# Performance work log

Hardware: AMD Instinct MI355X
Metric: run time of the kernel (lower is better)

Reference implementation:

```python
import jax, jax.numpy as jnp
import numpy as np

WS = (7, 7)   # window size
SS = (3, 3)   # shift size
NH = 8        # num heads
DIM = 256
B_, H_, W_ = 16, 112, 112


def _rel_index(wh, ww):
    ch, cw = np.meshgrid(np.arange(wh), np.arange(ww), indexing='ij')
    cf = np.stack([ch, cw]).reshape(2, -1)
    rc = (cf[:, :, None] - cf[:, None, :]).transpose(1, 2, 0)
    rc[:, :, 0] += wh - 1
    rc[:, :, 1] += ww - 1
    rc[:, :, 0] *= 2 * ww - 1
    return rc.sum(-1).reshape(-1)


def _shift_mask(pH, pW, wh, ww, sh, sw):
    m = np.zeros((pH, pW))
    cnt = 0
    for h0, h1 in ((0, pH - wh), (pH - wh, pH - sh), (pH - sh, pH)):
        for w0, w1 in ((0, pW - ww), (pW - ww, pW - sw), (pW - sw, pW)):
            m[h0:h1, w0:w1] = cnt
            cnt += 1
    m = m.reshape(pH // wh, wh, pW // ww, ww).transpose(0, 2, 1, 3).reshape(-1, wh * ww)
    d = m[:, None, :] - m[:, :, None]  # (nW, N, N), [w,i,j] = m[w,j]-m[w,i]
    return np.where(d != 0, -100.0, 0.0).astype(np.float32)


def _partition(x, wh, ww):
    B, H, W, C = x.shape
    x = x.reshape(B, H // wh, wh, W // ww, ww, C).transpose(0, 1, 3, 2, 4, 5)
    return x.reshape(B * (H // wh) * (W // ww), wh * ww, C)


def _unpartition(x, B, H, W, wh, ww):
    C = x.shape[-1]
    x = x.reshape(B, H // wh, W // ww, wh, ww, C).transpose(0, 1, 3, 2, 4, 5)
    return x.reshape(B, H, W, C)


def setup_inputs() -> dict:
    key = jax.random.key(0)
    ks = jax.random.split(key, 12)
    D = DIM
    inp = {
        'Q': jax.random.normal(ks[0], (B_, H_, W_, D), jnp.float32),
        'K': jax.random.normal(ks[1], (B_, H_, W_, D), jnp.float32),
        'V': jax.random.normal(ks[2], (B_, H_, W_, D), jnp.float32),
        'Qw': jax.random.normal(ks[3], (D, D), jnp.float32) * 0.02,
        'Qb': jax.random.normal(ks[4], (D,), jnp.float32) * 0.02,
        'Kw': jax.random.normal(ks[5], (D, D), jnp.float32) * 0.02,
        'Kb': jax.random.normal(ks[6], (D,), jnp.float32) * 0.02,
        'Vw': jax.random.normal(ks[7], (D, D), jnp.float32) * 0.02,
        'Vb': jax.random.normal(ks[8], (D,), jnp.float32) * 0.02,
        'Pw': jax.random.normal(ks[9], (D, D), jnp.float32) * 0.02,
        'Pb': jax.random.normal(ks[10], (D,), jnp.float32) * 0.02,
        'rpb_table': jax.random.normal(ks[11], ((2 * WS[0] - 1) * (2 * WS[1] - 1), NH), jnp.float32) * 0.02,
        'rp_index': jnp.asarray(_rel_index(WS[0], WS[1]), jnp.int32),
    }
    return inp


def reference(Q, K, V, Qw, Qb, Kw, Kb, Vw, Vb, Pw, Pb, rpb_table, rp_index):
    wh, ww = WS
    nh = NH
    B, H, W, C = Q.shape
    N = wh * ww
    hd = C // nh
    pad_b = (wh - H % wh) % wh
    pad_r = (ww - W % ww) % ww
    if pad_b or pad_r:
        pad = ((0, 0), (0, pad_b), (0, pad_r), (0, 0))
        Q, K, V = jnp.pad(Q, pad), jnp.pad(K, pad), jnp.pad(V, pad)
    pH, pW = H + pad_b, W + pad_r
    sh = 0 if wh >= pH else SS[0]
    sw = 0 if ww >= pW else SS[1]
    shifted = (sh + sw) > 0
    if shifted:
        Q = jnp.roll(Q, (-sh, -sw), (1, 2))
        K = jnp.roll(K, (-sh, -sw), (1, 2))
        V = jnp.roll(V, (-sh, -sw), (1, 2))
    xq = _partition(Q, wh, ww)  # (B*nW, N, C)
    xk = _partition(K, wh, ww)
    xv = _partition(V, wh, ww)
    q = (xq @ Qw.T + Qb).reshape(-1, N, nh, hd).transpose(0, 2, 1, 3) * (hd ** -0.5)
    k = (xk @ Kw.T + Kb).reshape(-1, N, nh, hd).transpose(0, 2, 1, 3)
    v = (xv @ Vw.T + Vb).reshape(-1, N, nh, hd).transpose(0, 2, 1, 3)
    bias = rpb_table[rp_index].reshape(N, N, nh).transpose(2, 0, 1)  # (nh, N, N)
    attn = jnp.einsum('bhnd,bhmd->bhnm', q, k) + bias[None]
    if shifted:
        mask = jnp.asarray(_shift_mask(pH, pW, wh, ww, sh, sw))  # (nW, N, N)
        nW = (pH // wh) * (pW // ww)
        attn = attn.reshape(B, nW, nh, N, N) + mask[None, :, None]
        attn = attn.reshape(-1, nh, N, N)
    attn = jax.nn.softmax(attn, axis=-1)
    x = jnp.einsum('bhnm,bhmd->bhnd', attn, v).transpose(0, 2, 1, 3).reshape(-1, N, C)
    x = x @ Pw.T + Pb
    x = _unpartition(x, B, pH, pW, wh, ww)
    if shifted:
        x = jnp.roll(x, (sh, sw), (1, 2))
    return x[:, :H, :W, :]
```

## Files before the change

### kernel.cpp

```cpp
#include <hip/hip_runtime.h>


typedef short  bf16x4_t __attribute__((ext_vector_type(4)));
typedef short  bf16x8_t __attribute__((ext_vector_type(8)));
typedef float  f32x4_t  __attribute__((ext_vector_type(4)));
typedef int    i32x4_t  __attribute__((ext_vector_type(4)));

#define HH    112
#define WWDIM 112
#define NTOK  49
#define NWIN  4096
#define SHIFT 3
#define LOG2E 1.4426950408889634f
#define MASKS (-144.26950408889634f)

__device__ __forceinline__ unsigned short f2bf(float f) {
  unsigned u = __builtin_bit_cast(unsigned, f);
  u += 0x7FFFu + ((u >> 16) & 1u);
  return (unsigned short)(u >> 16);
}

__device__ __forceinline__ unsigned cvtpk(float a, float b) {
  unsigned r;
  asm("v_cvt_pk_bf16_f32 %0, %1, %2" : "=v"(r) : "v"(a), "v"(b));
  return r;
}

__device__ __forceinline__ float exp2fast(float x) {
  float r;
  asm("v_exp_f32 %0, %1" : "=v"(r) : "v"(x));
  return r;
}

__device__ __forceinline__ bf16x8_t ld8(const unsigned short* p) {
  return __builtin_bit_cast(bf16x8_t, *reinterpret_cast<const i32x4_t*>(p));
}

__device__ __forceinline__ bf16x4_t pack4(float a, float b, float c, float d) {
  union { unsigned u[2]; bf16x4_t v; } t;
  t.u[0] = cvtpk(a, b); t.u[1] = cvtpk(c, d);
  return t.v;
}

__device__ __forceinline__ int swzi(int row, int col, int rowElems) {
  int by = col << 1;
  int sb = (((by >> 4) ^ (row & 7)) << 4) | (by & 15);
  return row * rowElems + (sb >> 1);
}

__global__ void prep_kernel(const float* __restrict__ Qw, const float* __restrict__ Kw,
                            const float* __restrict__ Vw, const float* __restrict__ Pw,
                            const float* __restrict__ rpb, const int* __restrict__ rpi,
                            unsigned short* __restrict__ wbf, float* __restrict__ biasP) {
  int idx = blockIdx.x * 256 + threadIdx.x;
  if (idx < 4 * 65536) {
    int which = idx >> 16, e = idx & 65535;
    const float* s = (which == 0) ? Qw : (which == 1) ? Kw : (which == 2) ? Vw : Pw;
    wbf[idx] = f2bf(s[e]);
  }
  if (idx < 8 * 49 * 64) {
    int h = idx / 3136, r = idx - h * 3136;
    int i = r >> 6, j = r & 63;
    biasP[idx] = (i < NTOK && j < NTOK) ? rpb[rpi[i * NTOK + j] * 8 + h] * LOG2E : 0.f;
  }
}

#define GLOAD(SRC)                                                            \
  do {                                                                        \
    _Pragma("unroll") for (int it = 0; it < 8; ++it) {                        \
      g[it] = ((wid + (it << 3)) < NTOK)                                      \
                  ? *reinterpret_cast<const float4*>((SRC) + goff[it])        \
                  : make_float4(0.f, 0.f, 0.f, 0.f);                          \
    }                                                                         \
  } while (0)

#define XWRITE(B)                                                             \
  do {                                                                        \
    _Pragma("unroll") for (int it = 0; it < 8; ++it) {                        \
      unsigned v0 = cvtpk(g[it].x, g[it].y);                                  \
      unsigned v1 = cvtpk(g[it].z, g[it].w);                                  \
      *reinterpret_cast<uint2*>(                                              \
          &Xs[B][swzi(wid + (it << 3), lane << 2, 256)]) = make_uint2(v0, v1);\
    }                                                                         \
  } while (0)

#define WHOIST(PH)                                                            \
  do {                                                                        \
    const unsigned short* W_ = wbf + ((PH) << 16);                            \
    _Pragma("unroll") for (int ks = 0; ks < 8; ++ks)                          \
        _Pragma("unroll") for (int t = 0; t < 2; ++t)                         \
            bw[ks][t] =                                                       \
        ld8(&W_[(((wid << 5) + (t << 4) + lo) << 8) + (ks << 5) + kof]);      \
  } while (0)

__global__ __launch_bounds__(512, 2) void fused_kernel(
    const float* __restrict__ Qin, const float* __restrict__ Kin, const float* __restrict__ Vin,
    const float* __restrict__ Qbv, const float* __restrict__ Kbv, const float* __restrict__ Vbv,
    const float* __restrict__ Pbv,
    const unsigned short* __restrict__ wbf, const float* __restrict__ biasP,
    float* __restrict__ out) {
  __shared__ unsigned short Xs[2][64 * 256];

  const int blk = blockIdx.x, tid = threadIdx.x;
  const int lane = tid & 63, wid = tid >> 6;
  const int b = blk >> 8, wi = (blk >> 4) & 15, wj = blk & 15;
  const int lo = lane & 15, hi = lane >> 4;
  const int g4 = hi << 2, kof = hi << 3;

  unsigned goff[8];
#pragma unroll
  for (int it = 0; it < 8; ++it) {
    int row = wid + (it << 3);
    unsigned off = 0;
    if (row < NTOK) {
      int i = row / 7, j = row - i * 7;
      int h_ = wi * 7 + i + SHIFT; if (h_ >= HH) h_ -= HH;
      int w_ = wj * 7 + j + SHIFT; if (w_ >= WWDIM) w_ -= WWDIM;
      off = ((unsigned)((b * HH + h_) * WWDIM + w_) << 8) + (lane << 2);
    }
    goff[it] = off;
  }

  float4 g[8];
  bf16x8_t bw[8][2];
  bf16x4_t qf[2][4], kf[2][4], vf[4][2];

  GLOAD(Qin);
  XWRITE(0);
  WHOIST(0);
  __syncthreads();

#pragma unroll
  for (int ph = 0; ph < 2; ++ph) {
    GLOAD(ph == 0 ? Kin : Vin);
    const unsigned short* Xb = Xs[ph];
    f32x4_t acc[2][4];
#pragma unroll
    for (int a = 0; a < 2; ++a)
#pragma unroll
      for (int c = 0; c < 4; ++c) acc[a][c] = (f32x4_t){0.f, 0.f, 0.f, 0.f};
#pragma unroll
    for (int ks = 0; ks < 8; ++ks) {
      const int kk = (ks << 5) + kof;
      bf16x8_t xb[4];
#pragma unroll
      for (int nj = 0; nj < 4; ++nj) xb[nj] = ld8(&Xb[swzi((nj << 4) + lo, kk, 256)]);
#pragma unroll
      for (int mi = 0; mi < 2; ++mi)
#pragma unroll
        for (int nj = 0; nj < 4; ++nj)
          acc[mi][nj] = __builtin_amdgcn_mfma_f32_16x16x32_bf16(bw[ks][mi], xb[nj], acc[mi][nj], 0, 0, 0);
    }
    const float* bias = (ph == 0) ? Qbv : Kbv;
    const float scale = (ph == 0) ? 0.17677669529663687f * LOG2E : 1.0f;
    bf16x4_t (*dst)[4] = (ph == 0) ? qf : kf;
#pragma unroll
    for (int mi = 0; mi < 2; ++mi) {
      const float4 bb = *reinterpret_cast<const float4*>(bias + (wid << 5) + (mi << 4) + g4);
#pragma unroll
      for (int nj = 0; nj < 4; ++nj)
        dst[mi][nj] = pack4((acc[mi][nj][0] + bb.x) * scale, (acc[mi][nj][1] + bb.y) * scale,
                            (acc[mi][nj][2] + bb.z) * scale, (acc[mi][nj][3] + bb.w) * scale);
    }
    XWRITE(ph ^ 1);
    WHOIST(ph + 1);
    __syncthreads();
  }

  {
    const unsigned short* Xb = Xs[0];
    f32x4_t acc[4][2];
#pragma unroll
    for (int a = 0; a < 4; ++a)
#pragma unroll
      for (int c = 0; c < 2; ++c) acc[a][c] = (f32x4_t){0.f, 0.f, 0.f, 0.f};
#pragma unroll
    for (int ks = 0; ks < 8; ++ks) {
      const int kk = (ks << 5) + kof;
      bf16x8_t xa[4];
#pragma unroll
      for (int mi = 0; mi < 4; ++mi) xa[mi] = ld8(&Xb[swzi((mi << 4) + lo, kk, 256)]);
#pragma unroll
      for (int mi = 0; mi < 4; ++mi)
#pragma unroll
        for (int t = 0; t < 2; ++t)
          acc[mi][t] = __builtin_amdgcn_mfma_f32_16x16x32_bf16(xa[mi], bw[ks][t], acc[mi][t], 0, 0, 0);
    }
    float bbv[2];
#pragma unroll
    for (int t = 0; t < 2; ++t) bbv[t] = Vbv[(wid << 5) + (t << 4) + lo];
#pragma unroll
    for (int mi = 0; mi < 4; ++mi)
#pragma unroll
      for (int t = 0; t < 2; ++t)
        vf[mi][t] = pack4(acc[mi][t][0] + bbv[t], acc[mi][t][1] + bbv[t],
                          acc[mi][t][2] + bbv[t], acc[mi][t][3] + bbv[t]);
  }
  WHOIST(3);

  const bool wi15 = (wi == 15), wj15 = (wj == 15);
  unsigned kbi = 0, kbj = 0, kval = 0;
#pragma unroll
  for (int njk = 0; njk < 4; ++njk)
#pragma unroll
    for (int rg = 0; rg < 4; ++rg) {
      int kt = (njk << 4) + g4 + rg;
      if (kt < NTOK) {
        int ti = kt / 7, tj = kt - (kt / 7) * 7;
        unsigned bit = 1u << (njk * 4 + rg);
        kval |= bit;
        if (ti >= 4) kbi |= bit;
        if (tj >= 4) kbj |= bit;
      }
    }

  bf16x4_t pf[4][4];
#pragma unroll
  for (int njq = 0; njq < 4; ++njq) {
    const int qt = (njq << 4) + lo;
    const bool qv = qt < NTOK;
    const int sqt = qv ? qt : 0;
    const float* bq = biasP + wid * 3136 + (sqt << 6);
    f32x4_t bfr[4];
#pragma unroll
    for (int njk = 0; njk < 4; ++njk)
      bfr[njk] = *reinterpret_cast<const f32x4_t*>(bq + (njk << 4) + g4);

    f32x4_t stc[4];
    __builtin_amdgcn_s_setprio(1);
#pragma unroll
    for (int njk = 0; njk < 4; ++njk) {
      stc[njk] = __builtin_amdgcn_mfma_f32_16x16x16bf16_1k(
          kf[0][njk], qf[0][njq], (f32x4_t){0.f, 0.f, 0.f, 0.f}, 0, 0, 0);
      stc[njk] = __builtin_amdgcn_mfma_f32_16x16x16bf16_1k(
          kf[1][njk], qf[1][njq], stc[njk], 0, 0, 0);
    }
    __builtin_amdgcn_s_setprio(0);

    const int qti = sqt / 7, qtj = sqt - (sqt / 7) * 7;
    const bool qbi = qti >= 4, qbj = qtj >= 4;
    float vals[4][4];
    float m = -3e38f;
#pragma unroll
    for (int njk = 0; njk < 4; ++njk)
#pragma unroll
      for (int rg = 0; rg < 4; ++rg) {
        const int bit = njk * 4 + rg;
        const bool valid = qv && ((kval >> bit) & 1u);
        float v = stc[njk][rg] + bfr[njk][rg];
        if (wi15 && (qbi != (bool)((kbi >> bit) & 1u))) v += MASKS;
        if (wj15 && (qbj != (bool)((kbj >> bit) & 1u))) v += MASKS;
        v = valid ? v : -1e30f;
        vals[njk][rg] = v;
        m = fmaxf(m, v);
      }
    m = fmaxf(m, __shfl_xor(m, 16));
    m = fmaxf(m, __shfl_xor(m, 32));
    float sum = 0.f;
#pragma unroll
    for (int njk = 0; njk < 4; ++njk)
#pragma unroll
      for (int rg = 0; rg < 4; ++rg) {
        const float e = exp2fast(vals[njk][rg] - m);
        vals[njk][rg] = e;
        sum += e;
      }
    sum += __shfl_xor(sum, 16);
    sum += __shfl_xor(sum, 32);
    const float inv = __builtin_amdgcn_rcpf(sum);
#pragma unroll
    for (int njk = 0; njk < 4; ++njk)
      pf[njk][njq] = pack4(vals[njk][0] * inv, vals[njk][1] * inv,
                           vals[njk][2] * inv, vals[njk][3] * inv);
  }

  f32x4_t o[2][4];
#pragma unroll
  for (int a = 0; a < 2; ++a)
#pragma unroll
    for (int c = 0; c < 4; ++c) o[a][c] = (f32x4_t){0.f, 0.f, 0.f, 0.f};
  __builtin_amdgcn_s_setprio(1);
#pragma unroll
  for (int mi = 0; mi < 4; ++mi)
#pragma unroll
    for (int t = 0; t < 2; ++t)
#pragma unroll
      for (int njq = 0; njq < 4; ++njq)
        o[t][njq] = __builtin_amdgcn_mfma_f32_16x16x16bf16_1k(vf[mi][t], pf[mi][njq], o[t][njq], 0, 0, 0);
  __builtin_amdgcn_s_setprio(0);

#pragma unroll
  for (int t = 0; t < 2; ++t)
#pragma unroll
    for (int njq = 0; njq < 4; ++njq) {
      const int qt = (njq << 4) + lo;
      const int ch0 = (wid << 5) + (t << 4) + g4;
      *reinterpret_cast<uint2*>(&Xs[1][swzi(qt, ch0, 256)]) =
          make_uint2(cvtpk(o[t][njq][0], o[t][njq][1]), cvtpk(o[t][njq][2], o[t][njq][3]));
    }
  __syncthreads();

  {
    const unsigned short* Xb = Xs[1];
    f32x4_t y[2][4];
#pragma unroll
    for (int a = 0; a < 2; ++a)
#pragma unroll
      for (int c = 0; c < 4; ++c) y[a][c] = (f32x4_t){0.f, 0.f, 0.f, 0.f};
#pragma unroll
    for (int ks = 0; ks < 8; ++ks) {
      const int kk = (ks << 5) + kof;
      bf16x8_t xb[4];
#pragma unroll
      for (int nj = 0; nj < 4; ++nj) xb[nj] = ld8(&Xb[swzi((nj << 4) + lo, kk, 256)]);
#pragma unroll
      for (int mi = 0; mi < 2; ++mi)
#pragma unroll
        for (int nj = 0; nj < 4; ++nj)
          y[mi][nj] = __builtin_amdgcn_mfma_f32_16x16x32_bf16(bw[ks][mi], xb[nj], y[mi][nj], 0, 0, 0);
    }
    float4 pb[2];
#pragma unroll
    for (int mi = 0; mi < 2; ++mi)
      pb[mi] = *reinterpret_cast<const float4*>(Pbv + (wid << 5) + (mi << 4) + g4);
#pragma unroll
    for (int nj = 0; nj < 4; ++nj) {
      const int tok = (nj << 4) + lo;
      if (tok < NTOK) {
        const int i = tok / 7, j = tok - (tok / 7) * 7;
        int h_ = wi * 7 + i + SHIFT; if (h_ >= HH) h_ -= HH;
        int w_ = wj * 7 + j + SHIFT; if (w_ >= WWDIM) w_ -= WWDIM;
        float* ob = out + ((size_t)((b * HH + h_) * WWDIM + w_) << 8);
#pragma unroll
        for (int mi = 0; mi < 2; ++mi) {
          const int ch0 = (wid << 5) + (mi << 4) + g4;
          *reinterpret_cast<float4*>(ob + ch0) =
              make_float4(y[mi][nj][0] + pb[mi].x, y[mi][nj][1] + pb[mi].y,
                          y[mi][nj][2] + pb[mi].z, y[mi][nj][3] + pb[mi].w);
        }
      }
    }
  }
}

extern "C" void kernel_launch(void* const* d_in, const int* in_sizes, int n_in,
                              void* d_out, int out_size, void* d_ws, size_t ws_size,
                              hipStream_t stream) {
  const float* Q   = (const float*)d_in[0];
  const float* K   = (const float*)d_in[1];
  const float* V   = (const float*)d_in[2];
  const float* Qw  = (const float*)d_in[3];
  const float* Qb  = (const float*)d_in[4];
  const float* Kw  = (const float*)d_in[5];
  const float* Kb  = (const float*)d_in[6];
  const float* Vw  = (const float*)d_in[7];
  const float* Vb  = (const float*)d_in[8];
  const float* Pw  = (const float*)d_in[9];
  const float* Pb  = (const float*)d_in[10];
  const float* rpb = (const float*)d_in[11];
  const int*   rpi = (const int*)d_in[12];

  unsigned short* wbf = (unsigned short*)d_ws;
  float* biasP = (float*)(wbf + 4 * 65536);

  const size_t need = (size_t)4 * 65536 * 2 + (size_t)8 * 49 * 64 * 4;
  if (ws_size < need) return;

  prep_kernel<<<1024, 256, 0, stream>>>(Qw, Kw, Vw, Pw, rpb, rpi, wbf, biasP);
  fused_kernel<<<NWIN, 512, 0, stream>>>(Q, K, V, Qb, Kb, Vb, Pb, wbf, biasP,
                                         (float*)d_out);
}
```

Before: 448.2 us.

## Halve block to four waves, each owning two heads, stream weights per k-step

The fused window-attention kernel now launches 256 threads per window instead of 512. Each wave computes 64 output channels (two heads) rather than 32. The whole weight slice is no longer hoisted into registers per phase. Instead it is double-buffered one k-step at a time from global/L2 inside each projection loop. This is meant to cut the per-window wave count and the register pressure of holding full weight tiles. In exchange each wave does twice the MFMA work serially, and weight loads may add latency inside the GEMM loops.

```diff
diff --git a/kernel.cpp b/kernel.cpp
--- a/kernel.cpp
+++ b/kernel.cpp
@@ -67,8 +67,8 @@
 
 #define GLOAD(SRC)                                                            \
   do {                                                                        \
-    _Pragma("unroll") for (int it = 0; it < 8; ++it) {                        \
-      g[it] = ((wid + (it << 3)) < NTOK)                                      \
+    _Pragma("unroll") for (int it = 0; it < 16; ++it) {                       \
+      g[it] = (((it << 2) + wid) < NTOK)                                      \
                   ? *reinterpret_cast<const float4*>((SRC) + goff[it])        \
                   : make_float4(0.f, 0.f, 0.f, 0.f);                          \
     }                                                                         \
@@ -76,24 +76,22 @@
 
 #define XWRITE(B)                                                             \
   do {                                                                        \
-    _Pragma("unroll") for (int it = 0; it < 8; ++it) {                        \
+    _Pragma("unroll") for (int it = 0; it < 16; ++it) {                       \
       unsigned v0 = cvtpk(g[it].x, g[it].y);                                  \
       unsigned v1 = cvtpk(g[it].z, g[it].w);                                  \
       *reinterpret_cast<uint2*>(                                              \
-          &Xs[B][swzi(wid + (it << 3), lane << 2, 256)]) = make_uint2(v0, v1);\
+          &Xs[B][swzi((it << 2) + wid, lane << 2, 256)]) = make_uint2(v0, v1);\
     }                                                                         \
   } while (0)
 
-#define WHOIST(PH)                                                            \
+#define WLOAD(WP, KS, S)                                                      \
   do {                                                                        \
-    const unsigned short* W_ = wbf + ((PH) << 16);                            \
-    _Pragma("unroll") for (int ks = 0; ks < 8; ++ks)                          \
-        _Pragma("unroll") for (int t = 0; t < 2; ++t)                         \
-            bw[ks][t] =                                                       \
-        ld8(&W_[(((wid << 5) + (t << 4) + lo) << 8) + (ks << 5) + kof]);      \
+    _Pragma("unroll") for (int m = 0; m < 4; ++m)                             \
+      bwr[S][m] = ld8(&(WP)[(((wid << 6) + (m << 4) + lo) << 8) +             \
+                            ((KS) << 5) + kof]);                              \
   } while (0)
 
-__global__ __launch_bounds__(512, 2) void fused_kernel(
+__global__ __launch_bounds__(256, 2) void fused_kernel(
     const float* __restrict__ Qin, const float* __restrict__ Kin, const float* __restrict__ Vin,
     const float* __restrict__ Qbv, const float* __restrict__ Kbv, const float* __restrict__ Vbv,
     const float* __restrict__ Pbv,
@@ -107,10 +105,10 @@
   const int lo = lane & 15, hi = lane >> 4;
   const int g4 = hi << 2, kof = hi << 3;
 
-  unsigned goff[8];
-#pragma unroll
-  for (int it = 0; it < 8; ++it) {
-    int row = wid + (it << 3);
+  unsigned goff[16];
+#pragma unroll
+  for (int it = 0; it < 16; ++it) {
+    int row = (it << 2) + wid;
     unsigned off = 0;
     if (row < NTOK) {
       int i = row / 7, j = row - i * 7;
@@ -121,61 +119,66 @@
     goff[it] = off;
   }
 
-  float4 g[8];
-  bf16x8_t bw[8][2];
-  bf16x4_t qf[2][4], kf[2][4], vf[4][2];
+  float4 g[16];
+  bf16x8_t bwr[2][4];
+  bf16x4_t qf[4][4], kf[4][4], vf[4][4];
 
   GLOAD(Qin);
   XWRITE(0);
-  WHOIST(0);
   __syncthreads();
 
 #pragma unroll
   for (int ph = 0; ph < 2; ++ph) {
     GLOAD(ph == 0 ? Kin : Vin);
     const unsigned short* Xb = Xs[ph];
-    f32x4_t acc[2][4];
-#pragma unroll
-    for (int a = 0; a < 2; ++a)
+    const unsigned short* W_ = wbf + (ph << 16);
+    f32x4_t acc[4][4];
+#pragma unroll
+    for (int a = 0; a < 4; ++a)
 #pragma unroll
       for (int c = 0; c < 4; ++c) acc[a][c] = (f32x4_t){0.f, 0.f, 0.f, 0.f};
+    WLOAD(W_, 0, 0);
 #pragma unroll
     for (int ks = 0; ks < 8; ++ks) {
+      if (ks < 7) WLOAD(W_, ks + 1, (ks + 1) & 1);
       const int kk = (ks << 5) + kof;
       bf16x8_t xb[4];
 #pragma unroll
       for (int nj = 0; nj < 4; ++nj) xb[nj] = ld8(&Xb[swzi((nj << 4) + lo, kk, 256)]);
 #pragma unroll
-      for (int mi = 0; mi < 2; ++mi)
+      for (int m = 0; m < 4; ++m)
 #pragma unroll
         for (int nj = 0; nj < 4; ++nj)
-          acc[mi][nj] = __builtin_amdgcn_mfma_f32_16x16x32_bf16(bw[ks][mi], xb[nj], acc[mi][nj], 0, 0, 0);
+          acc[m][nj] = __builtin_amdgcn_mfma_f32_16x16x32_bf16(bwr[ks & 1][m], xb[nj], acc[m][nj], 0, 0, 0);
     }
     const float* bias = (ph == 0) ? Qbv : Kbv;
     const float scale = (ph == 0) ? 0.17677669529663687f * LOG2E : 1.0f;
-    bf16x4_t (*dst)[4] = (ph == 0) ? qf : kf;
-#pragma unroll
-    for (int mi = 0; mi < 2; ++mi) {
-      const float4 bb = *reinterpret_cast<const float4*>(bias + (wid << 5) + (mi << 4) + g4);
-#pragma unroll
-      for (int nj = 0; nj < 4; ++nj)
-        dst[mi][nj] = pack4((acc[mi][nj][0] + bb.x) * scale, (acc[mi][nj][1] + bb.y) * scale,
-                            (acc[mi][nj][2] + bb.z) * scale, (acc[mi][nj][3] + bb.w) * scale);
+#pragma unroll
+    for (int m = 0; m < 4; ++m) {
+      const float4 bb = *reinterpret_cast<const float4*>(bias + (wid << 6) + (m << 4) + g4);
+#pragma unroll
+      for (int nj = 0; nj < 4; ++nj) {
+        const bf16x4_t v = pack4((acc[m][nj][0] + bb.x) * scale, (acc[m][nj][1] + bb.y) * scale,
+                                 (acc[m][nj][2] + bb.z) * scale, (acc[m][nj][3] + bb.w) * scale);
+        if (ph == 0) qf[m][nj] = v; else kf[m][nj] = v;
+      }
     }
     XWRITE(ph ^ 1);
-    WHOIST(ph + 1);
     __syncthreads();
   }
 
   {
     const unsigned short* Xb = Xs[0];
-    f32x4_t acc[4][2];
+    const unsigned short* W_ = wbf + (2 << 16);
+    f32x4_t acc[4][4];
 #pragma unroll
     for (int a = 0; a < 4; ++a)
 #pragma unroll
-      for (int c = 0; c < 2; ++c) acc[a][c] = (f32x4_t){0.f, 0.f, 0.f, 0.f};
+      for (int c = 0; c < 4; ++c) acc[a][c] = (f32x4_t){0.f, 0.f, 0.f, 0.f};
+    WLOAD(W_, 0, 0);
 #pragma unroll
     for (int ks = 0; ks < 8; ++ks) {
+      if (ks < 7) WLOAD(W_, ks + 1, (ks + 1) & 1);
       const int kk = (ks << 5) + kof;
       bf16x8_t xa[4];
 #pragma unroll
@@ -183,20 +186,19 @@
 #pragma unroll
       for (int mi = 0; mi < 4; ++mi)
 #pragma unroll
-        for (int t = 0; t < 2; ++t)
-          acc[mi][t] = __builtin_amdgcn_mfma_f32_16x16x32_bf16(xa[mi], bw[ks][t], acc[mi][t], 0, 0, 0);
-    }
-    float bbv[2];
-#pragma unroll
-    for (int t = 0; t < 2; ++t) bbv[t] = Vbv[(wid << 5) + (t << 4) + lo];
+        for (int t = 0; t < 4; ++t)
+          acc[mi][t] = __builtin_amdgcn_mfma_f32_16x16x32_bf16(xa[mi], bwr[ks & 1][t], acc[mi][t], 0, 0, 0);
+    }
+    float bbv[4];
+#pragma unroll
+    for (int t = 0; t < 4; ++t) bbv[t] = Vbv[(wid << 6) + (t << 4) + lo];
 #pragma unroll
     for (int mi = 0; mi < 4; ++mi)
 #pragma unroll
-      for (int t = 0; t < 2; ++t)
+      for (int t = 0; t < 4; ++t)
         vf[mi][t] = pack4(acc[mi][t][0] + bbv[t], acc[mi][t][1] + bbv[t],
                           acc[mi][t][2] + bbv[t], acc[mi][t][3] + bbv[t]);
   }
-  WHOIST(3);
 
   const bool wi15 = (wi == 15), wj15 = (wj == 15);
   unsigned kbi = 0, kbj = 0, kval = 0;
@@ -214,115 +216,121 @@
       }
     }
 
-  bf16x4_t pf[4][4];
-#pragma unroll
-  for (int njq = 0; njq < 4; ++njq) {
-    const int qt = (njq << 4) + lo;
-    const bool qv = qt < NTOK;
-    const int sqt = qv ? qt : 0;
-    const float* bq = biasP + wid * 3136 + (sqt << 6);
-    f32x4_t bfr[4];
-#pragma unroll
-    for (int njk = 0; njk < 4; ++njk)
-      bfr[njk] = *reinterpret_cast<const f32x4_t*>(bq + (njk << 4) + g4);
-
-    f32x4_t stc[4];
-    __builtin_amdgcn_s_setprio(1);
-#pragma unroll
-    for (int njk = 0; njk < 4; ++njk) {
-      stc[njk] = __builtin_amdgcn_mfma_f32_16x16x16bf16_1k(
-          kf[0][njk], qf[0][njq], (f32x4_t){0.f, 0.f, 0.f, 0.f}, 0, 0, 0);
-      stc[njk] = __builtin_amdgcn_mfma_f32_16x16x16bf16_1k(
-          kf[1][njk], qf[1][njq], stc[njk], 0, 0, 0);
-    }
-    __builtin_amdgcn_s_setprio(0);
-
-    const int qti = sqt / 7, qtj = sqt - (sqt / 7) * 7;
-    const bool qbi = qti >= 4, qbj = qtj >= 4;
-    float vals[4][4];
-    float m = -3e38f;
-#pragma unroll
-    for (int njk = 0; njk < 4; ++njk)
-#pragma unroll
-      for (int rg = 0; rg < 4; ++rg) {
-        const int bit = njk * 4 + rg;
-        const bool valid = qv && ((kval >> bit) & 1u);
-        float v = stc[njk][rg] + bfr[njk][rg];
-        if (wi15 && (qbi != (bool)((kbi >> bit) & 1u))) v += MASKS;
-        if (wj15 && (qbj != (bool)((kbj >> bit) & 1u))) v += MASKS;
-        v = valid ? v : -1e30f;
-        vals[njk][rg] = v;
-        m = fmaxf(m, v);
-      }
-    m = fmaxf(m, __shfl_xor(m, 16));
-    m = fmaxf(m, __shfl_xor(m, 32));
-    float sum = 0.f;
-#pragma unroll
-    for (int njk = 0; njk < 4; ++njk)
-#pragma unroll
-      for (int rg = 0; rg < 4; ++rg) {
-        const float e = exp2fast(vals[njk][rg] - m);
-        vals[njk][rg] = e;
-        sum += e;
-      }
-    sum += __shfl_xor(sum, 16);
-    sum += __shfl_xor(sum, 32);
-    const float inv = __builtin_amdgcn_rcpf(sum);
-#pragma unroll
-    for (int njk = 0; njk < 4; ++njk)
-      pf[njk][njq] = pack4(vals[njk][0] * inv, vals[njk][1] * inv,
-                           vals[njk][2] * inv, vals[njk][3] * inv);
-  }
-
-  f32x4_t o[2][4];
-#pragma unroll
-  for (int a = 0; a < 2; ++a)
-#pragma unroll
-    for (int c = 0; c < 4; ++c) o[a][c] = (f32x4_t){0.f, 0.f, 0.f, 0.f};
-  __builtin_amdgcn_s_setprio(1);
-#pragma unroll
-  for (int mi = 0; mi < 4; ++mi)
-#pragma unroll
-    for (int t = 0; t < 2; ++t)
-#pragma unroll
-      for (int njq = 0; njq < 4; ++njq)
-        o[t][njq] = __builtin_amdgcn_mfma_f32_16x16x16bf16_1k(vf[mi][t], pf[mi][njq], o[t][njq], 0, 0, 0);
-  __builtin_amdgcn_s_setprio(0);
-
-#pragma unroll
-  for (int t = 0; t < 2; ++t)
+#pragma unroll
+  for (int hh = 0; hh < 2; ++hh) {
+    const int h = (wid << 1) + hh;
+    const int co = h << 5;
+
+    bf16x4_t pf[4][4];
 #pragma unroll
     for (int njq = 0; njq < 4; ++njq) {
       const int qt = (njq << 4) + lo;
-      const int ch0 = (wid << 5) + (t << 4) + g4;
-      *reinterpret_cast<uint2*>(&Xs[1][swzi(qt, ch0, 256)]) =
-          make_uint2(cvtpk(o[t][njq][0], o[t][njq][1]), cvtpk(o[t][njq][2], o[t][njq][3]));
-    }
+      const bool qv = qt < NTOK;
+      const int sqt = qv ? qt : 0;
+      const float* bq = biasP + h * 3136 + (sqt << 6);
+      f32x4_t bfr[4];
+#pragma unroll
+      for (int njk = 0; njk < 4; ++njk)
+        bfr[njk] = *reinterpret_cast<const f32x4_t*>(bq + (njk << 4) + g4);
+
+      f32x4_t stc[4];
+      __builtin_amdgcn_s_setprio(1);
+#pragma unroll
+      for (int njk = 0; njk < 4; ++njk) {
+        stc[njk] = __builtin_amdgcn_mfma_f32_16x16x16bf16_1k(
+            kf[(hh << 1)][njk], qf[(hh << 1)][njq], (f32x4_t){0.f, 0.f, 0.f, 0.f}, 0, 0, 0);
+        stc[njk] = __builtin_amdgcn_mfma_f32_16x16x16bf16_1k(
+            kf[(hh << 1) + 1][njk], qf[(hh << 1) + 1][njq], stc[njk], 0, 0, 0);
+      }
+      __builtin_amdgcn_s_setprio(0);
+
+      const int qti = sqt / 7, qtj = sqt - (sqt / 7) * 7;
+      const bool qbi = qti >= 4, qbj = qtj >= 4;
+      float m = -3e38f;
+#pragma unroll
+      for (int njk = 0; njk < 4; ++njk)
+#pragma unroll
+        for (int rg = 0; rg < 4; ++rg) {
+          const int bit = njk * 4 + rg;
+          const bool valid = qv && ((kval >> bit) & 1u);
+          float v = stc[njk][rg] + bfr[njk][rg];
+          if (wi15 && (qbi != (bool)((kbi >> bit) & 1u))) v += MASKS;
+          if (wj15 && (qbj != (bool)((kbj >> bit) & 1u))) v += MASKS;
+          v = valid ? v : -1e30f;
+          stc[njk][rg] = v;
+          m = fmaxf(m, v);
+        }
+      m = fmaxf(m, __shfl_xor(m, 16));
+      m = fmaxf(m, __shfl_xor(m, 32));
+      float sum = 0.f;
+#pragma unroll
+      for (int njk = 0; njk < 4; ++njk)
+#pragma unroll
+        for (int rg = 0; rg < 4; ++rg) {
+          const float e = exp2fast(stc[njk][rg] - m);
+          stc[njk][rg] = e;
+          sum += e;
+        }
+      sum += __shfl_xor(sum, 16);
+      sum += __shfl_xor(sum, 32);
+      const float inv = __builtin_amdgcn_rcpf(sum);
+#pragma unroll
+      for (int njk = 0; njk < 4; ++njk)
+        pf[njk][njq] = pack4(stc[njk][0] * inv, stc[njk][1] * inv,
+                             stc[njk][2] * inv, stc[njk][3] * inv);
+    }
+
+    f32x4_t o[2][4];
+#pragma unroll
+    for (int a = 0; a < 2; ++a)
+#pragma unroll
+      for (int c = 0; c < 4; ++c) o[a][c] = (f32x4_t){0.f, 0.f, 0.f, 0.f};
+    __builtin_amdgcn_s_setprio(1);
+#pragma unroll
+    for (int mi = 0; mi < 4; ++mi)
+#pragma unroll
+      for (int t2 = 0; t2 < 2; ++t2)
+#pragma unroll
+        for (int njq = 0; njq < 4; ++njq)
+          o[t2][njq] = __builtin_amdgcn_mfma_f32_16x16x16bf16_1k(
+              vf[mi][(hh << 1) + t2], pf[mi][njq], o[t2][njq], 0, 0, 0);
+    __builtin_amdgcn_s_setprio(0);
+
+#pragma unroll
+    for (int t2 = 0; t2 < 2; ++t2)
+#pragma unroll
+      for (int njq = 0; njq < 4; ++njq) {
+        const int qt = (njq << 4) + lo;
+        const int ch0 = co + (t2 << 4) + g4;
+        *reinterpret_cast<uint2*>(&Xs[1][swzi(qt, ch0, 256)]) =
+            make_uint2(cvtpk(o[t2][njq][0], o[t2][njq][1]),
+                       cvtpk(o[t2][njq][2], o[t2][njq][3]));
+      }
+  }
   __syncthreads();
 
   {
     const unsigned short* Xb = Xs[1];
-    f32x4_t y[2][4];
-#pragma unroll
-    for (int a = 0; a < 2; ++a)
+    const unsigned short* W_ = wbf + (3 << 16);
+    f32x4_t y[4][4];
+#pragma unroll
+    for (int a = 0; a < 4; ++a)
 #pragma unroll
       for (int c = 0; c < 4; ++c) y[a][c] = (f32x4_t){0.f, 0.f, 0.f, 0.f};
+    WLOAD(W_, 0, 0);
 #pragma unroll
     for (int ks = 0; ks < 8; ++ks) {
+      if (ks < 7) WLOAD(W_, ks + 1, (ks + 1) & 1);
       const int kk = (ks << 5) + kof;
       bf16x8_t xb[4];
 #pragma unroll
       for (int nj = 0; nj < 4; ++nj) xb[nj] = ld8(&Xb[swzi((nj << 4) + lo, kk, 256)]);
 #pragma unroll
-      for (int mi = 0; mi < 2; ++mi)
+      for (int m = 0; m < 4; ++m)
 #pragma unroll
         for (int nj = 0; nj < 4; ++nj)
-          y[mi][nj] = __builtin_amdgcn_mfma_f32_16x16x32_bf16(bw[ks][mi], xb[nj], y[mi][nj], 0, 0, 0);
-    }
-    float4 pb[2];
-#pragma unroll
-    for (int mi = 0; mi < 2; ++mi)
-      pb[mi] = *reinterpret_cast<const float4*>(Pbv + (wid << 5) + (mi << 4) + g4);
+          y[m][nj] = __builtin_amdgcn_mfma_f32_16x16x32_bf16(bwr[ks & 1][m], xb[nj], y[m][nj], 0, 0, 0);
+    }
 #pragma unroll
     for (int nj = 0; nj < 4; ++nj) {
       const int tok = (nj << 4) + lo;
@@ -332,11 +340,12 @@
         int w_ = wj * 7 + j + SHIFT; if (w_ >= WWDIM) w_ -= WWDIM;
         float* ob = out + ((size_t)((b * HH + h_) * WWDIM + w_) << 8);
 #pragma unroll
-        for (int mi = 0; mi < 2; ++mi) {
-          const int ch0 = (wid << 5) + (mi << 4) + g4;
+        for (int m = 0; m < 4; ++m) {
+          const int ch0 = (wid << 6) + (m << 4) + g4;
+          const float4 pb = *reinterpret_cast<const float4*>(Pbv + ch0);
           *reinterpret_cast<float4*>(ob + ch0) =
-              make_float4(y[mi][nj][0] + pb[mi].x, y[mi][nj][1] + pb[mi].y,
-                          y[mi][nj][2] + pb[mi].z, y[mi][nj][3] + pb[mi].w);
+              make_float4(y[m][nj][0] + pb.x, y[m][nj][1] + pb.y,
+                          y[m][nj][2] + pb.z, y[m][nj][3] + pb.w);
         }
       }
     }
@@ -367,6 +376,6 @@
   if (ws_size < need) return;
 
   prep_kernel<<<1024, 256, 0, stream>>>(Qw, Kw, Vw, Pw, rpb, rpi, wbf, biasP);
-  fused_kernel<<<NWIN, 512, 0, stream>>>(Q, K, V, Qb, Kb, Vb, Pb, wbf, biasP,
+  fused_kernel<<<NWIN, 256, 0, stream>>>(Q, K, V, Qb, Kb, Vb, Pb, wbf, biasP,
                                          (float*)d_out);
 }
```

New measurement: 445.5 us. Within noise of the previous version (-0.6%).
